# Kernel optimization log

Hardware: AMD Instinct MI355X
Metric: run time of the kernel (lower is better)

The kernel has to match this reference:

```python
import jax, jax.numpy as jnp
import numpy as np

N = 50000   # nodes
E = 800000  # edges (avg degree 16)
D = 128     # in_dim == out_dim
EPS = 1e-5  # LayerNorm eps (torch default)


def setup_inputs() -> dict:
    key = jax.random.key(0)
    ks = jax.random.split(key, 8)
    x = jax.random.normal(ks[0], (N, D), dtype=jnp.float32)
    edge_row = jax.random.randint(ks[1], (E,), 0, N, dtype=jnp.int32)
    edge_col = jax.random.randint(ks[2], (E,), 0, N, dtype=jnp.int32)
    edge_val = jax.random.uniform(ks[3], (E,), dtype=jnp.float32)
    W = jax.random.normal(ks[4], (D, D), dtype=jnp.float32) / np.sqrt(D).astype(np.float32)
    b = jnp.zeros((D,), jnp.float32)
    gamma = jnp.ones((D,), jnp.float32)
    beta = jnp.zeros((D,), jnp.float32)
    return {"x": x, "edge_val": edge_val, "W": W, "b": b,
            "gamma": gamma, "beta": beta,
            "edge_row": edge_row, "edge_col": edge_col}


def reference(x, edge_val, W, b, gamma, beta, edge_row, edge_col):
    # SpMM: support = adj @ x, adj in COO form (row, col, val)
    msgs = edge_val[:, None] * x[edge_col]                      # [E, D] gather
    support = jax.ops.segment_sum(msgs, edge_row, num_segments=x.shape[0])  # [N, D]
    # Linear (torch stores weight as [out, in])
    h = support @ W.T + b                                       # [N, D]
    # LayerNorm over last dim
    mu = jnp.mean(h, axis=-1, keepdims=True)
    var = jnp.mean(jnp.square(h - mu), axis=-1, keepdims=True)
    h = (h - mu) * jax.lax.rsqrt(var + EPS) * gamma + beta
    # ReLU; dropout is identity at inference
    return jax.nn.relu(h)
```

## Files before the change

### kernel.cpp

```cpp
#include <hip/hip_runtime.h>

#define D 128
#define LN_EPS 1e-5f
#define RPB 16
#define POISON 0xAAAAAAAAu
#define ECAP 68
#define EMAX 64
#define KBB 256
#define KBT 1024
#define DCAP 3200
#define NFB 4096
#define XST_STRIDE 68

typedef __attribute__((ext_vector_type(8))) short short8;
typedef __attribute__((ext_vector_type(4))) float f32x4;

union FragU { uint4 u; short8 s; };

__device__ __forceinline__ unsigned bf16_hi(float f) {
    unsigned u = __float_as_uint(f);
    return (u + 0x7FFFu + ((u >> 16) & 1u)) & 0xFFFF0000u;
}
__device__ __forceinline__ float lo16f(unsigned u) { return __uint_as_float(u << 16); }
__device__ __forceinline__ float hi16f(unsigned u) { return __uint_as_float(u & 0xFFFF0000u); }

__global__ void __launch_bounds__(KBT) prep_kernel(
    const int* __restrict__ edge_row, const int* __restrict__ edge_col,
    const float* __restrict__ edge_val, const float* __restrict__ W,
    const float* __restrict__ x, unsigned* __restrict__ yb16,
    uint2* __restrict__ binbuf, int* __restrict__ tab,
    int E, int N, int epb) {
    __shared__ __align__(16) char arena[50176];
    uint2* dense = (uint2*)arena;
    int*   cnt   = (int*)(arena + 25600);
    int (*tmp)[KBT] = (int(*)[KBT])(arena + 41984);
    unsigned* wbL = (unsigned*)arena;
    typedef unsigned XstRow[XST_STRIDE];
    XstRow* xstA = (XstRow*)(arena + 32768);
    int t = threadIdx.x;
    int blk = blockIdx.x;

    for (int i = t; i < NFB; i += KBT) cnt[i] = 0;
    __syncthreads();

    int e0 = blk * epb;
    int e1 = e0 + epb; if (e1 > E) e1 = E;
    int nume = e1 - e0; if (nume < 0) nume = 0;
    int quadEnd = e0 + (nume & ~3);

    for (int i = e0 + t * 4; i + 3 < e1; i += KBT * 4) {
        int4 r = *(const int4*)(edge_row + i);
        atomicAdd(&cnt[r.x >> 4], 1);
        atomicAdd(&cnt[r.y >> 4], 1);
        atomicAdd(&cnt[r.z >> 4], 1);
        atomicAdd(&cnt[r.w >> 4], 1);
    }
    for (int i = quadEnd + t; i < e1; i += KBT) atomicAdd(&cnt[edge_row[i] >> 4], 1);
    __syncthreads();

    {
        int i0 = t * 4;
        int a0 = cnt[i0], a1 = cnt[i0 + 1], a2 = cnt[i0 + 2], a3 = cnt[i0 + 3];
        int s1 = a0 + a1, s2 = s1 + a2, tot = s2 + a3;
        tmp[0][t] = tot;
        __syncthreads();
        int buf = 0;
        for (int off = 1; off < KBT; off <<= 1) {
            int v = tmp[buf][t];
            if (t >= off) v += tmp[buf][t - off];
            tmp[1 - buf][t] = v;
            buf ^= 1;
            __syncthreads();
        }
        int base = tmp[buf][t] - tot;
        cnt[i0] = base; cnt[i0 + 1] = base + a0;
        cnt[i0 + 2] = base + s1; cnt[i0 + 3] = base + s2;
    }
    __syncthreads();

    for (int i = t; i < NFB; i += KBT) tab[blk * NFB + i] = cnt[i];
    __syncthreads();

    for (int i = e0 + t * 4; i + 3 < e1; i += KBT * 4) {
        int4 r = *(const int4*)(edge_row + i);
        int4 c = *(const int4*)(edge_col + i);
        float4 v = *(const float4*)(edge_val + i);
        int p0 = atomicAdd(&cnt[r.x >> 4], 1);
        int p1 = atomicAdd(&cnt[r.y >> 4], 1);
        int p2 = atomicAdd(&cnt[r.z >> 4], 1);
        int p3 = atomicAdd(&cnt[r.w >> 4], 1);
        dense[p0] = make_uint2(((unsigned)c.x << 16) | (unsigned)(r.x & 15), bf16_hi(v.x));
        dense[p1] = make_uint2(((unsigned)c.y << 16) | (unsigned)(r.y & 15), bf16_hi(v.y));
        dense[p2] = make_uint2(((unsigned)c.z << 16) | (unsigned)(r.z & 15), bf16_hi(v.z));
        dense[p3] = make_uint2(((unsigned)c.w << 16) | (unsigned)(r.w & 15), bf16_hi(v.w));
    }
    for (int i = quadEnd + t; i < e1; i += KBT) {
        int r = edge_row[i];
        int p = atomicAdd(&cnt[r >> 4], 1);
        dense[p] = make_uint2(((unsigned)edge_col[i] << 16) | (unsigned)(r & 15),
                              bf16_hi(edge_val[i]));
    }
    __syncthreads();

    for (int i = t; i < nume; i += KBT)
        binbuf[(size_t)blk * DCAP + i] = dense[i];
    __syncthreads();

    for (int i = t; i < 8192; i += KBT) {
        int u  = i & 3;
        int L  = (i >> 2) & 63;
        int nt = (i >> 8) & 7;
        int kt = i >> 11;
        int n = nt * 16 + (L & 15);
        int k = kt * 32 + (L >> 4) * 8 + u * 2;
        wbL[i] = bf16_hi(W[n * D + k + 1]) | (bf16_hi(W[n * D + k]) >> 16);
    }
    __syncthreads();

    {
        int T = (N + RPB - 1) / RPB;
        int g = t >> 8;
        int tg = t & 255;
        XstRow* xst = xstA + g * RPB;
        for (int tb0 = blk * 4; tb0 < T; tb0 += gridDim.x * 4) {
            int tile = tb0 + g;
            if (tile < T) {
                int r = tg >> 4, q = tg & 15;
                int row = tile * RPB + r;
                uint4 o = make_uint4(0u, 0u, 0u, 0u);
                if (row < N) {
                    float4 a = *(const float4*)(x + (size_t)row * D + q * 8);
                    float4 c = *(const float4*)(x + (size_t)row * D + q * 8 + 4);
                    o.x = bf16_hi(a.y) | (bf16_hi(a.x) >> 16);
                    o.y = bf16_hi(a.w) | (bf16_hi(a.z) >> 16);
                    o.z = bf16_hi(c.y) | (bf16_hi(c.x) >> 16);
                    o.w = bf16_hi(c.w) | (bf16_hi(c.z) >> 16);
                }
                *(uint4*)&xst[r][q * 4] = o;
            }
            __syncthreads();
            if (tile < T) {
                int L = tg & 63;
                int w = tg >> 6;
                int m = L & 15;
                int gk = L >> 4;
                f32x4 acc0 = {0.f, 0.f, 0.f, 0.f};
                f32x4 acc1 = {0.f, 0.f, 0.f, 0.f};
#pragma unroll
                for (int kt = 0; kt < 4; ++kt) {
                    FragU a, b0, b1;
                    a.u  = *(const uint4*)&xst[m][kt * 16 + gk * 4];
                    b0.u = *(const uint4*)(wbL + (((size_t)(kt * 8 + w * 2)) * 64 + L) * 4);
                    b1.u = *(const uint4*)(wbL + (((size_t)(kt * 8 + w * 2 + 1)) * 64 + L) * 4);
                    acc0 = __builtin_amdgcn_mfma_f32_16x16x32_bf16(a.s, b0.s, acc0, 0, 0, 0);
                    acc1 = __builtin_amdgcn_mfma_f32_16x16x32_bf16(a.s, b1.s, acc1, 0, 0, 0);
                }
                bool evenm = (m & 1) == 0;
#pragma unroll
                for (int i = 0; i < 4; ++i) {
                    float p0 = __shfl_xor(acc0[i], 1);
                    float p1 = __shfl_xor(acc1[i], 1);
                    if (evenm) {
                        int row = tile * RPB + gk * 4 + i;
                        if (row < N) {
                            unsigned y0 = bf16_hi(p0) | (bf16_hi(acc0[i]) >> 16);
                            unsigned y1 = bf16_hi(p1) | (bf16_hi(acc1[i]) >> 16);
                            size_t base = (size_t)row * (D / 2) + w * 16 + (m >> 1);
                            yb16[base] = y0;
                            yb16[base + 8] = y1;
                        }
                    }
                }
            }
            __syncthreads();
        }
    }
}

__global__ void __launch_bounds__(256) fused_lite(
    const unsigned* __restrict__ yb16, const uint2* __restrict__ binbuf,
    const int* __restrict__ tab,
    const float* __restrict__ bias, const float* __restrict__ gamma,
    const float* __restrict__ beta, float* __restrict__ out, int N) {
    __shared__ unsigned ecol[RPB][ECAP];
    __shared__ int ecnt[RPB];
    __shared__ int pdeg[RPB];
    int t = threadIdx.x;

    int nwg = (int)gridDim.x;
    int swq = nwg >> 3, swr = nwg & 7;
    int xcd = (int)blockIdx.x & 7;
    int f = (xcd < swr ? xcd * (swq + 1) : swr * (swq + 1) + (xcd - swr) * swq)
          + ((int)blockIdx.x >> 3);
    int row0 = f * RPB;

    if (t < RPB) ecnt[t] = 0;
    int s = tab[t * NFB + f];
    int e = tab[t * NFB + f + 1];
    __syncthreads();

    {
        const uint2* bp = binbuf + (size_t)t * DCAP;
        for (int idx = s; idx < e; ++idx) {
            uint2 rec = bp[idx];
            int rl = (int)(rec.x & 15u);
            int p = atomicAdd(&ecnt[rl], 1);
            if (p < EMAX) ecol[rl][p] = rec.y | (rec.x >> 16);
        }
    }
    __syncthreads();
    if (t < RPB) {
        int c = ecnt[t]; if (c > EMAX) c = EMAX;
        int pe = (c + 3) & ~3;
        for (int k = c; k < pe; ++k) ecol[t][k] = 0;
        pdeg[t] = pe;
    }
    __syncthreads();

    {
        int r = t >> 4;
        int qd = t & 15;
        int row = row0 + r;
        float4 accA = make_float4(0.f, 0.f, 0.f, 0.f);
        float4 accB = make_float4(0.f, 0.f, 0.f, 0.f);
        if (row < N) {
            int pd = pdeg[r];
            const unsigned* yb = yb16 + qd * 4;
            for (int e4 = 0; e4 < pd; e4 += 4) {
                uint4 p = *(const uint4*)&ecol[r][e4];
                unsigned c0 = p.x & 0xFFFFu, c1 = p.y & 0xFFFFu;
                unsigned c2 = p.z & 0xFFFFu, c3 = p.w & 0xFFFFu;
                float w0 = __uint_as_float(p.x & 0xFFFF0000u);
                float w1 = __uint_as_float(p.y & 0xFFFF0000u);
                float w2 = __uint_as_float(p.z & 0xFFFF0000u);
                float w3 = __uint_as_float(p.w & 0xFFFF0000u);
                uint4 X0 = *(const uint4*)(yb + (size_t)c0 * (D / 2));
                uint4 X1 = *(const uint4*)(yb + (size_t)c1 * (D / 2));
                uint4 X2 = *(const uint4*)(yb + (size_t)c2 * (D / 2));
                uint4 X3 = *(const uint4*)(yb + (size_t)c3 * (D / 2));
                accA.x = fmaf(w0, lo16f(X0.x), accA.x);
                accA.y = fmaf(w0, hi16f(X0.x), accA.y);
                accA.z = fmaf(w0, lo16f(X0.y), accA.z);
                accA.w = fmaf(w0, hi16f(X0.y), accA.w);
                accB.x = fmaf(w0, lo16f(X0.z), accB.x);
                accB.y = fmaf(w0, hi16f(X0.z), accB.y);
                accB.z = fmaf(w0, lo16f(X0.w), accB.z);
                accB.w = fmaf(w0, hi16f(X0.w), accB.w);
                accA.x = fmaf(w1, lo16f(X1.x), accA.x);
                accA.y = fmaf(w1, hi16f(X1.x), accA.y);
                accA.z = fmaf(w1, lo16f(X1.y), accA.z);
                accA.w = fmaf(w1, hi16f(X1.y), accA.w);
                accB.x = fmaf(w1, lo16f(X1.z), accB.x);
                accB.y = fmaf(w1, hi16f(X1.z), accB.y);
                accB.z = fmaf(w1, lo16f(X1.w), accB.z);
                accB.w = fmaf(w1, hi16f(X1.w), accB.w);
                accA.x = fmaf(w2, lo16f(X2.x), accA.x);
                accA.y = fmaf(w2, hi16f(X2.x), accA.y);
                accA.z = fmaf(w2, lo16f(X2.y), accA.z);
                accA.w = fmaf(w2, hi16f(X2.y), accA.w);
                accB.x = fmaf(w2, lo16f(X2.z), accB.x);
                accB.y = fmaf(w2, hi16f(X2.z), accB.y);
                accB.z = fmaf(w2, lo16f(X2.w), accB.z);
                accB.w = fmaf(w2, hi16f(X2.w), accB.w);
                accA.x = fmaf(w3, lo16f(X3.x), accA.x);
                accA.y = fmaf(w3, hi16f(X3.x), accA.y);
                accA.z = fmaf(w3, lo16f(X3.y), accA.z);
                accA.w = fmaf(w3, hi16f(X3.y), accA.w);
                accB.x = fmaf(w3, lo16f(X3.z), accB.x);
                accB.y = fmaf(w3, hi16f(X3.z), accB.y);
                accB.z = fmaf(w3, lo16f(X3.w), accB.z);
                accB.w = fmaf(w3, hi16f(X3.w), accB.w);
            }
        }
        float4 bA = *(const float4*)(bias + qd * 8);
        float4 bB = *(const float4*)(bias + qd * 8 + 4);
        accA.x += bA.x; accA.y += bA.y; accA.z += bA.z; accA.w += bA.w;
        accB.x += bB.x; accB.y += bB.y; accB.z += bB.z; accB.w += bB.w;

        float sum = accA.x + accA.y + accA.z + accA.w
                  + accB.x + accB.y + accB.z + accB.w;
        float sq = accA.x * accA.x;
        sq = fmaf(accA.y, accA.y, sq);
        sq = fmaf(accA.z, accA.z, sq);
        sq = fmaf(accA.w, accA.w, sq);
        sq = fmaf(accB.x, accB.x, sq);
        sq = fmaf(accB.y, accB.y, sq);
        sq = fmaf(accB.z, accB.z, sq);
        sq = fmaf(accB.w, accB.w, sq);
#pragma unroll
        for (int off = 8; off > 0; off >>= 1) {
            sum += __shfl_xor(sum, off, 16);
            sq  += __shfl_xor(sq, off, 16);
        }
        float mu = sum * (1.0f / D);
        float var = sq * (1.0f / D) - mu * mu;
        float inv = rsqrtf(var + LN_EPS);

        if (row < N) {
            float4 gA = *(const float4*)(gamma + qd * 8);
            float4 gB = *(const float4*)(gamma + qd * 8 + 4);
            float4 eA = *(const float4*)(beta + qd * 8);
            float4 eB = *(const float4*)(beta + qd * 8 + 4);
            float4 oA, oB;
            oA.x = fmaxf((accA.x - mu) * inv * gA.x + eA.x, 0.f);
            oA.y = fmaxf((accA.y - mu) * inv * gA.y + eA.y, 0.f);
            oA.z = fmaxf((accA.z - mu) * inv * gA.z + eA.z, 0.f);
            oA.w = fmaxf((accA.w - mu) * inv * gA.w + eA.w, 0.f);
            oB.x = fmaxf((accB.x - mu) * inv * gB.x + eB.x, 0.f);
            oB.y = fmaxf((accB.y - mu) * inv * gB.y + eB.y, 0.f);
            oB.z = fmaxf((accB.z - mu) * inv * gB.z + eB.z, 0.f);
            oB.w = fmaxf((accB.w - mu) * inv * gB.w + eB.w, 0.f);
            *(float4*)(out + (size_t)row * D + qd * 8) = oA;
            *(float4*)(out + (size_t)row * D + qd * 8 + 4) = oB;
        }
    }
}

extern "C" void kernel_launch(void* const* d_in, const int* in_sizes, int n_in,
                              void* d_out, int out_size, void* d_ws, size_t ws_size,
                              hipStream_t stream) {
    const float* x        = (const float*)d_in[0];
    const float* edge_val = (const float*)d_in[1];
    const float* W        = (const float*)d_in[2];
    const float* b        = (const float*)d_in[3];
    const float* gamma    = (const float*)d_in[4];
    const float* beta     = (const float*)d_in[5];
    const int*   edge_row = (const int*)d_in[6];
    const int*   edge_col = (const int*)d_in[7];

    const int N = in_sizes[0] / D;
    const int E = in_sizes[1];
    const int T = (N + RPB - 1) / RPB;

    char* ws = (char*)d_ws;
    uint2*    binbuf = (uint2*)ws;    ws += (size_t)KBB * DCAP * sizeof(uint2);
    int*      tab    = (int*)ws;      ws += (size_t)KBB * NFB * sizeof(int);
    unsigned* yb16   = (unsigned*)ws; ws += (size_t)N * (D / 2) * sizeof(unsigned);

    int epb = ((E + KBB - 1) / KBB + 3) & ~3;

    prep_kernel<<<KBB, KBT, 0, stream>>>(edge_row, edge_col, edge_val, W, x,
                                         yb16, binbuf, tab, E, N, epb);
    fused_lite<<<T, 256, 0, stream>>>(yb16, binbuf, tab, b, gamma, beta,
                                      (float*)d_out, N);
}
```

Before: 135.3 us.

## Alternate GEMM and binning phase order per block; one wave per row tile

The prep kernel now runs the x@W GEMM and the edge-binning phases in opposite order on even and odd blocks, so blocks working at the same time stress different resources (compute/DRAM reads versus LDS atomics). The GEMM is also restructured: each wave owns a whole 16-row tile, loads its x fragments straight from global memory into registers, and computes all 8 output column tiles. This removes the LDS staging buffer for x and its barriers. In exchange it needs more accumulator registers, and it assumes the grid has enough waves to cover every tile in a single pass, since the grid-stride loop is gone.

```diff
diff --git a/kernel.cpp b/kernel.cpp
--- a/kernel.cpp
+++ b/kernel.cpp
@@ -10,7 +10,6 @@
 #define KBT 1024
 #define DCAP 3200
 #define NFB 4096
-#define XST_STRIDE 68
 
 typedef __attribute__((ext_vector_type(8))) short short8;
 typedef __attribute__((ext_vector_type(4))) float f32x4;
@@ -20,6 +19,9 @@
 __device__ __forceinline__ unsigned bf16_hi(float f) {
     unsigned u = __float_as_uint(f);
     return (u + 0x7FFFu + ((u >> 16) & 1u)) & 0xFFFF0000u;
+}
+__device__ __forceinline__ unsigned bfpack(float lo, float hi) {
+    return bf16_hi(hi) | (bf16_hi(lo) >> 16);
 }
 __device__ __forceinline__ float lo16f(unsigned u) { return __uint_as_float(u << 16); }
 __device__ __forceinline__ float hi16f(unsigned u) { return __uint_as_float(u & 0xFFFF0000u); }
@@ -35,143 +37,144 @@
     int*   cnt   = (int*)(arena + 25600);
     int (*tmp)[KBT] = (int(*)[KBT])(arena + 41984);
     unsigned* wbL = (unsigned*)arena;
-    typedef unsigned XstRow[XST_STRIDE];
-    XstRow* xstA = (XstRow*)(arena + 32768);
     int t = threadIdx.x;
     int blk = blockIdx.x;
 
-    for (int i = t; i < NFB; i += KBT) cnt[i] = 0;
-    __syncthreads();
-
-    int e0 = blk * epb;
-    int e1 = e0 + epb; if (e1 > E) e1 = E;
-    int nume = e1 - e0; if (nume < 0) nume = 0;
-    int quadEnd = e0 + (nume & ~3);
-
-    for (int i = e0 + t * 4; i + 3 < e1; i += KBT * 4) {
-        int4 r = *(const int4*)(edge_row + i);
-        atomicAdd(&cnt[r.x >> 4], 1);
-        atomicAdd(&cnt[r.y >> 4], 1);
-        atomicAdd(&cnt[r.z >> 4], 1);
-        atomicAdd(&cnt[r.w >> 4], 1);
-    }
-    for (int i = quadEnd + t; i < e1; i += KBT) atomicAdd(&cnt[edge_row[i] >> 4], 1);
-    __syncthreads();
-
-    {
-        int i0 = t * 4;
-        int a0 = cnt[i0], a1 = cnt[i0 + 1], a2 = cnt[i0 + 2], a3 = cnt[i0 + 3];
-        int s1 = a0 + a1, s2 = s1 + a2, tot = s2 + a3;
-        tmp[0][t] = tot;
-        __syncthreads();
-        int buf = 0;
-        for (int off = 1; off < KBT; off <<= 1) {
-            int v = tmp[buf][t];
-            if (t >= off) v += tmp[buf][t - off];
-            tmp[1 - buf][t] = v;
-            buf ^= 1;
-            __syncthreads();
-        }
-        int base = tmp[buf][t] - tot;
-        cnt[i0] = base; cnt[i0 + 1] = base + a0;
-        cnt[i0 + 2] = base + s1; cnt[i0 + 3] = base + s2;
-    }
-    __syncthreads();
-
-    for (int i = t; i < NFB; i += KBT) tab[blk * NFB + i] = cnt[i];
-    __syncthreads();
-
-    for (int i = e0 + t * 4; i + 3 < e1; i += KBT * 4) {
-        int4 r = *(const int4*)(edge_row + i);
-        int4 c = *(const int4*)(edge_col + i);
-        float4 v = *(const float4*)(edge_val + i);
-        int p0 = atomicAdd(&cnt[r.x >> 4], 1);
-        int p1 = atomicAdd(&cnt[r.y >> 4], 1);
-        int p2 = atomicAdd(&cnt[r.z >> 4], 1);
-        int p3 = atomicAdd(&cnt[r.w >> 4], 1);
-        dense[p0] = make_uint2(((unsigned)c.x << 16) | (unsigned)(r.x & 15), bf16_hi(v.x));
-        dense[p1] = make_uint2(((unsigned)c.y << 16) | (unsigned)(r.y & 15), bf16_hi(v.y));
-        dense[p2] = make_uint2(((unsigned)c.z << 16) | (unsigned)(r.z & 15), bf16_hi(v.z));
-        dense[p3] = make_uint2(((unsigned)c.w << 16) | (unsigned)(r.w & 15), bf16_hi(v.w));
-    }
-    for (int i = quadEnd + t; i < e1; i += KBT) {
-        int r = edge_row[i];
-        int p = atomicAdd(&cnt[r >> 4], 1);
-        dense[p] = make_uint2(((unsigned)edge_col[i] << 16) | (unsigned)(r & 15),
-                              bf16_hi(edge_val[i]));
-    }
-    __syncthreads();
-
-    for (int i = t; i < nume; i += KBT)
-        binbuf[(size_t)blk * DCAP + i] = dense[i];
-    __syncthreads();
-
-    for (int i = t; i < 8192; i += KBT) {
-        int u  = i & 3;
-        int L  = (i >> 2) & 63;
-        int nt = (i >> 8) & 7;
-        int kt = i >> 11;
-        int n = nt * 16 + (L & 15);
-        int k = kt * 32 + (L >> 4) * 8 + u * 2;
-        wbL[i] = bf16_hi(W[n * D + k + 1]) | (bf16_hi(W[n * D + k]) >> 16);
-    }
-    __syncthreads();
-
-    {
-        int T = (N + RPB - 1) / RPB;
-        int g = t >> 8;
-        int tg = t & 255;
-        XstRow* xst = xstA + g * RPB;
-        for (int tb0 = blk * 4; tb0 < T; tb0 += gridDim.x * 4) {
-            int tile = tb0 + g;
-            if (tile < T) {
-                int r = tg >> 4, q = tg & 15;
-                int row = tile * RPB + r;
-                uint4 o = make_uint4(0u, 0u, 0u, 0u);
+    bool gemmFirst = (blk & 1) == 0;
+    for (int ph = 0; ph < 2; ++ph) {
+        if ((ph == 0) == gemmFirst) {
+            for (int i = t; i < 8192; i += KBT) {
+                int u  = i & 3;
+                int L  = (i >> 2) & 63;
+                int nt = (i >> 8) & 7;
+                int kt = i >> 11;
+                int n = nt * 16 + (L & 15);
+                int k = kt * 32 + (L >> 4) * 8 + u * 2;
+                wbL[i] = bfpack(W[n * D + k], W[n * D + k + 1]);
+            }
+            __syncthreads();
+
+            int T = (N + RPB - 1) / RPB;
+            int wv = blk * (KBT / 64) + (t >> 6);
+            int L = t & 63;
+            int m = L & 15;
+            int g = L >> 4;
+            if (wv < T) {
+                int tile = wv;
+                int row = tile * RPB + m;
+                unsigned af[4][4];
                 if (row < N) {
-                    float4 a = *(const float4*)(x + (size_t)row * D + q * 8);
-                    float4 c = *(const float4*)(x + (size_t)row * D + q * 8 + 4);
-                    o.x = bf16_hi(a.y) | (bf16_hi(a.x) >> 16);
-                    o.y = bf16_hi(a.w) | (bf16_hi(a.z) >> 16);
-                    o.z = bf16_hi(c.y) | (bf16_hi(c.x) >> 16);
-                    o.w = bf16_hi(c.w) | (bf16_hi(c.z) >> 16);
+                    const float* xr = x + (size_t)row * D + g * 8;
+#pragma unroll
+                    for (int kt = 0; kt < 4; ++kt) {
+                        float4 a = *(const float4*)(xr + kt * 32);
+                        float4 c = *(const float4*)(xr + kt * 32 + 4);
+                        af[kt][0] = bfpack(a.x, a.y);
+                        af[kt][1] = bfpack(a.z, a.w);
+                        af[kt][2] = bfpack(c.x, c.y);
+                        af[kt][3] = bfpack(c.z, c.w);
+                    }
+                } else {
+#pragma unroll
+                    for (int kt = 0; kt < 4; ++kt)
+                        af[kt][0] = af[kt][1] = af[kt][2] = af[kt][3] = 0u;
                 }
-                *(uint4*)&xst[r][q * 4] = o;
-            }
-            __syncthreads();
-            if (tile < T) {
-                int L = tg & 63;
-                int w = tg >> 6;
-                int m = L & 15;
-                int gk = L >> 4;
-                f32x4 acc0 = {0.f, 0.f, 0.f, 0.f};
-                f32x4 acc1 = {0.f, 0.f, 0.f, 0.f};
+                f32x4 acc[8];
+#pragma unroll
+                for (int nt = 0; nt < 8; ++nt) acc[nt] = (f32x4){0.f, 0.f, 0.f, 0.f};
 #pragma unroll
                 for (int kt = 0; kt < 4; ++kt) {
-                    FragU a, b0, b1;
-                    a.u  = *(const uint4*)&xst[m][kt * 16 + gk * 4];
-                    b0.u = *(const uint4*)(wbL + (((size_t)(kt * 8 + w * 2)) * 64 + L) * 4);
-                    b1.u = *(const uint4*)(wbL + (((size_t)(kt * 8 + w * 2 + 1)) * 64 + L) * 4);
-                    acc0 = __builtin_amdgcn_mfma_f32_16x16x32_bf16(a.s, b0.s, acc0, 0, 0, 0);
-                    acc1 = __builtin_amdgcn_mfma_f32_16x16x32_bf16(a.s, b1.s, acc1, 0, 0, 0);
+                    FragU a;
+                    a.u = make_uint4(af[kt][0], af[kt][1], af[kt][2], af[kt][3]);
+#pragma unroll
+                    for (int nt = 0; nt < 8; ++nt) {
+                        FragU b;
+                        b.u = *(const uint4*)(wbL + (((size_t)(kt * 8 + nt)) * 64 + L) * 4);
+                        acc[nt] = __builtin_amdgcn_mfma_f32_16x16x32_bf16(a.s, b.s, acc[nt], 0, 0, 0);
+                    }
                 }
                 bool evenm = (m & 1) == 0;
 #pragma unroll
-                for (int i = 0; i < 4; ++i) {
-                    float p0 = __shfl_xor(acc0[i], 1);
-                    float p1 = __shfl_xor(acc1[i], 1);
-                    if (evenm) {
-                        int row = tile * RPB + gk * 4 + i;
-                        if (row < N) {
-                            unsigned y0 = bf16_hi(p0) | (bf16_hi(acc0[i]) >> 16);
-                            unsigned y1 = bf16_hi(p1) | (bf16_hi(acc1[i]) >> 16);
-                            size_t base = (size_t)row * (D / 2) + w * 16 + (m >> 1);
-                            yb16[base] = y0;
-                            yb16[base + 8] = y1;
+                for (int nt = 0; nt < 8; ++nt) {
+#pragma unroll
+                    for (int i = 0; i < 4; ++i) {
+                        float p = __shfl_xor(acc[nt][i], 1);
+                        if (evenm) {
+                            int ro = tile * RPB + g * 4 + i;
+                            if (ro < N)
+                                yb16[(size_t)ro * (D / 2) + nt * 8 + (m >> 1)] =
+                                    bf16_hi(p) | (bf16_hi(acc[nt][i]) >> 16);
                         }
                     }
                 }
             }
+            __syncthreads();
+        } else {
+            for (int i = t; i < NFB; i += KBT) cnt[i] = 0;
+            __syncthreads();
+
+            int e0 = blk * epb;
+            int e1 = e0 + epb; if (e1 > E) e1 = E;
+            int nume = e1 - e0; if (nume < 0) nume = 0;
+            int quadEnd = e0 + (nume & ~3);
+
+            for (int i = e0 + t * 4; i + 3 < e1; i += KBT * 4) {
+                int4 r = *(const int4*)(edge_row + i);
+                atomicAdd(&cnt[r.x >> 4], 1);
+                atomicAdd(&cnt[r.y >> 4], 1);
+                atomicAdd(&cnt[r.z >> 4], 1);
+                atomicAdd(&cnt[r.w >> 4], 1);
+            }
+            for (int i = quadEnd + t; i < e1; i += KBT)
+                atomicAdd(&cnt[edge_row[i] >> 4], 1);
+            __syncthreads();
+
+            {
+                int i0 = t * 4;
+                int a0 = cnt[i0], a1 = cnt[i0 + 1], a2 = cnt[i0 + 2], a3 = cnt[i0 + 3];
+                int s1 = a0 + a1, s2 = s1 + a2, tot = s2 + a3;
+                tmp[0][t] = tot;
+                __syncthreads();
+                int buf = 0;
+                for (int off = 1; off < KBT; off <<= 1) {
+                    int v = tmp[buf][t];
+                    if (t >= off) v += tmp[buf][t - off];
+                    tmp[1 - buf][t] = v;
+                    buf ^= 1;
+                    __syncthreads();
+                }
+                int base = tmp[buf][t] - tot;
+                cnt[i0] = base; cnt[i0 + 1] = base + a0;
+                cnt[i0 + 2] = base + s1; cnt[i0 + 3] = base + s2;
+            }
+            __syncthreads();
+
+            for (int i = t; i < NFB; i += KBT) tab[blk * NFB + i] = cnt[i];
+            __syncthreads();
+
+            for (int i = e0 + t * 4; i + 3 < e1; i += KBT * 4) {
+                int4 r = *(const int4*)(edge_row + i);
+                int4 c = *(const int4*)(edge_col + i);
+                float4 v = *(const float4*)(edge_val + i);
+                int p0 = atomicAdd(&cnt[r.x >> 4], 1);
+                int p1 = atomicAdd(&cnt[r.y >> 4], 1);
+                int p2 = atomicAdd(&cnt[r.z >> 4], 1);
+                int p3 = atomicAdd(&cnt[r.w >> 4], 1);
+                dense[p0] = make_uint2(((unsigned)c.x << 16) | (unsigned)(r.x & 15), bf16_hi(v.x));
+                dense[p1] = make_uint2(((unsigned)c.y << 16) | (unsigned)(r.y & 15), bf16_hi(v.y));
+                dense[p2] = make_uint2(((unsigned)c.z << 16) | (unsigned)(r.z & 15), bf16_hi(v.z));
+                dense[p3] = make_uint2(((unsigned)c.w << 16) | (unsigned)(r.w & 15), bf16_hi(v.w));
+            }
+            for (int i = quadEnd + t; i < e1; i += KBT) {
+                int r = edge_row[i];
+                int p = atomicAdd(&cnt[r >> 4], 1);
+                dense[p] = make_uint2(((unsigned)edge_col[i] << 16) | (unsigned)(r & 15),
+                                      bf16_hi(edge_val[i]));
+            }
+            __syncthreads();
+
+            for (int i = t; i < nume; i += KBT)
+                binbuf[(size_t)blk * DCAP + i] = dense[i];
             __syncthreads();
         }
     }
```

After: 136.7 us. No clear change (+1.0%).
